# Optimization experiments

Hardware: AMD Instinct MI355X
Metric: run time of the kernel (lower is better)

## Reference

```python
import jax, jax.numpy as jnp
import numpy as np

B, S = 64, 256           # batch, seq_len
V, E = 50000, 256        # vocab, embedding dim
H, L = 256, 9            # lstm hidden, num labels


def setup_inputs() -> dict:
    key = jax.random.key(0)
    ks = jax.random.split(key, 12)
    inputs = jax.random.randint(ks[0], (B, S), 0, V, dtype=jnp.int32)
    attention_mask = jnp.ones((B, S), dtype=jnp.int32)
    label = jax.random.randint(ks[1], (B, S), 0, L, dtype=jnp.int32)
    emb = jax.random.normal(ks[2], (V, E), jnp.float32) * 0.02
    # LSTM weights, keras gate order: i, f, g(cell), o stacked along last axis
    W_fwd = jax.random.normal(ks[3], (E, 4 * H), jnp.float32) * 0.05
    U_fwd = jax.random.normal(ks[4], (H, 4 * H), jnp.float32) * 0.05
    b_fwd = jnp.zeros((4 * H,), jnp.float32)
    W_bwd = jax.random.normal(ks[5], (E, 4 * H), jnp.float32) * 0.05
    U_bwd = jax.random.normal(ks[6], (H, 4 * H), jnp.float32) * 0.05
    b_bwd = jnp.zeros((4 * H,), jnp.float32)
    W_dense = jax.random.normal(ks[7], (2 * H, L), jnp.float32) * 0.05
    b_dense = jnp.zeros((L,), jnp.float32)
    trans = jax.random.uniform(ks[8], (L, L), jnp.float32)  # tf.random.uniform init
    return dict(inputs=inputs, attention_mask=attention_mask, label=label,
                emb=emb, W_fwd=W_fwd, U_fwd=U_fwd, b_fwd=b_fwd,
                W_bwd=W_bwd, U_bwd=U_bwd, b_bwd=b_bwd,
                W_dense=W_dense, b_dense=b_dense, trans=trans)


def _lstm(x, W, U, b):
    # x: [B,S,E] -> h sequence [B,S,H]; keras default activations (sigmoid/tanh)
    Bx = x.shape[0]
    Hd = U.shape[0]
    xz = jnp.einsum('bse,ef->bsf', x, W) + b  # precompute input projection

    def step(carry, zt):
        h, c = carry
        z = zt + h @ U
        i, f, g, o = jnp.split(z, 4, axis=-1)
        c = jax.nn.sigmoid(f) * c + jax.nn.sigmoid(i) * jnp.tanh(g)
        h = jax.nn.sigmoid(o) * jnp.tanh(c)
        return (h, c), h

    init = (jnp.zeros((Bx, Hd), x.dtype), jnp.zeros((Bx, Hd), x.dtype))
    _, hs = jax.lax.scan(step, init, jnp.swapaxes(xz, 0, 1))
    return jnp.swapaxes(hs, 0, 1)


def _crf_log_likelihood(logits, tags, lengths, trans):
    # logits [B,S,L], tags [B,S] int, lengths [B] int, trans [L,L]
    Bx, Sx, Lx = logits.shape
    t_idx = jnp.arange(Sx)
    valid = (t_idx[None, :] < lengths[:, None]).astype(logits.dtype)  # [B,S]
    unary = jnp.take_along_axis(logits, tags[..., None], axis=-1)[..., 0]
    unary_score = jnp.sum(unary * valid, axis=1)
    pair_valid = (t_idx[None, :Sx - 1] < (lengths[:, None] - 1)).astype(logits.dtype)
    binary = trans[tags[:, :-1], tags[:, 1:]]
    binary_score = jnp.sum(binary * pair_valid, axis=1)

    # forward algorithm (log-space), masked so alpha is carried through padding
    alpha0 = logits[:, 0]  # [B,L]

    def step(alpha, inp):
        emit, m = inp  # emit [B,L], m [B] bool
        new = jax.nn.logsumexp(alpha[:, :, None] + trans[None], axis=1) + emit
        alpha = jnp.where(m[:, None], new, alpha)
        return alpha, None

    emits = jnp.swapaxes(logits[:, 1:], 0, 1)               # [S-1,B,L]
    masks = jnp.swapaxes(t_idx[None, 1:] < lengths[:, None], 0, 1)
    alpha, _ = jax.lax.scan(step, alpha0, (emits, masks))
    log_norm = jax.nn.logsumexp(alpha, axis=-1)
    return unary_score + binary_score - log_norm


def reference(inputs, attention_mask, label, emb, W_fwd, U_fwd, b_fwd,
              W_bwd, U_bwd, b_bwd, W_dense, b_dense, trans):
    x = emb[inputs]  # [B,S,E]; dropout is identity at inference (training=None)
    h_f = _lstm(x, W_fwd, U_fwd, b_fwd)
    h_b = _lstm(x[:, ::-1], W_bwd, U_bwd, b_bwd)[:, ::-1]
    h = jnp.concatenate([h_f, h_b], axis=-1)  # [B,S,2H]
    logits = h @ W_dense + b_dense            # [B,S,L]
    lengths = jnp.sum((attention_mask != 0).astype(jnp.int32), axis=1)
    log_likelihood = _crf_log_likelihood(logits, label, lengths, trans)
    return logits, log_likelihood, trans
```

## Files before the change

kernel.cpp:

```cpp
#include <hip/hip_runtime.h>
#include <hip/hip_fp16.h>

typedef _Float16 half2_t __attribute__((ext_vector_type(2)));
typedef unsigned int u32;

constexpr int Bn = 64, Sn = 256, Ln = 9;
constexpr int G4H = 1024;

constexpr size_t XZ_OFF   = 0;
constexpr size_t XZ_BYTES = (size_t)2 * Bn * Sn * G4H * 4;
constexpr size_t H_OFF    = XZ_OFF + XZ_BYTES;
constexpr size_t H_BYTES  = (size_t)Bn * Sn * 512 * 4;
constexpr size_t UPK_OFF  = H_OFF + H_BYTES;
constexpr size_t UPK_BYTES= (size_t)2 * 128 * G4H * 4;

__device__ __forceinline__ float sigf(float x) {
  return __fdividef(1.0f, 1.0f + __expf(-x));
}
__device__ __forceinline__ float tanhf_fast(float x) {
  x = fminf(fmaxf(x, -15.0f), 15.0f);
  float e = __expf(-2.0f * x);
  return __fdividef(1.0f - e, 1.0f + e);
}

#if __has_builtin(__builtin_amdgcn_fdot2)
__device__ __forceinline__ float FDOT2(half2_t a, half2_t b, float c) {
  return __builtin_amdgcn_fdot2(a, b, c, false);
}
#else
__device__ __forceinline__ float FDOT2(half2_t a, half2_t b, float c) {
  return c + (float)a.x * (float)b.x + (float)a.y * (float)b.y;
}
#endif

__device__ __forceinline__ half2_t H2(u32 w) { return __builtin_bit_cast(half2_t, w); }
__device__ __forceinline__ half2_t H2F(float f) { return __builtin_bit_cast(half2_t, f); }

__global__ void pack_u(const float* __restrict__ Uf, const float* __restrict__ Ub,
                       u32* __restrict__ upk) {
  int idx = blockIdx.x * 256 + threadIdx.x;
  if (idx >= 2 * 128 * 1024) return;
  int d  = idx >> 17;
  int kp = (idx >> 10) & 127;
  int j  = idx & 1023;
  const float* U = d ? Ub : Uf;
  _Float16 a = (_Float16)U[(size_t)(2 * kp) * 1024 + j];
  _Float16 b = (_Float16)U[(size_t)(2 * kp + 1) * 1024 + j];
  u32 pa = (u32)__builtin_bit_cast(unsigned short, a);
  u32 pb = (u32)__builtin_bit_cast(unsigned short, b);
  upk[idx] = pa | (pb << 16);
}

__global__ __launch_bounds__(256, 4)
void xz_gemm(const int* __restrict__ tok, const float* __restrict__ emb,
             const float* __restrict__ Wf, const float* __restrict__ biasf,
             const float* __restrict__ Wb, const float* __restrict__ biasb,
             float* __restrict__ xz) {
  __shared__ float As[32][64];
  __shared__ float Bs[32][128];
  __shared__ int toks[64];
  const int tid = threadIdx.x;
  const int mt = blockIdx.x, nt = blockIdx.y;
  const int d = nt >> 3;
  const float* W    = d ? Wb : Wf;
  const float* bias = d ? biasb : biasf;
  const int n0 = (nt & 7) * 128;
  const int r0 = mt * 64;
  if (tid < 64) toks[tid] = tok[r0 + tid];
  __syncthreads();
  const int tr = tid >> 4, tc = tid & 15;
  float acc[4][8];
#pragma unroll
  for (int j = 0; j < 8; ++j) {
    float bv = bias[n0 + tc * 8 + j];
#pragma unroll
    for (int i = 0; i < 4; ++i) acc[i][j] = bv;
  }
  const int ai = tid >> 2, kq = tid & 3;
  const int kb = tid >> 3, fb = tid & 7;
  for (int k0 = 0; k0 < 256; k0 += 32) {
    const float* ar = emb + (size_t)toks[ai] * 256 + k0 + kq * 8;
    float4 a0 = *(const float4*)ar;
    float4 a1 = *(const float4*)(ar + 4);
    As[kq * 8 + 0][ai] = a0.x; As[kq * 8 + 1][ai] = a0.y;
    As[kq * 8 + 2][ai] = a0.z; As[kq * 8 + 3][ai] = a0.w;
    As[kq * 8 + 4][ai] = a1.x; As[kq * 8 + 5][ai] = a1.y;
    As[kq * 8 + 6][ai] = a1.z; As[kq * 8 + 7][ai] = a1.w;
    const float* wr = W + (size_t)(k0 + kb) * 1024 + n0;
#pragma unroll
    for (int q = 0; q < 4; ++q)
      *(float4*)&Bs[kb][(fb + 8 * q) * 4] = *(const float4*)(wr + (fb + 8 * q) * 4);
    __syncthreads();
#pragma unroll
    for (int kk = 0; kk < 32; ++kk) {
      float4 a4 = *(const float4*)&As[kk][tr * 4];
      float4 b0 = *(const float4*)&Bs[kk][tc * 8];
      float4 b1 = *(const float4*)&Bs[kk][tc * 8 + 4];
      float av[4] = {a4.x, a4.y, a4.z, a4.w};
      float bv[8] = {b0.x, b0.y, b0.z, b0.w, b1.x, b1.y, b1.z, b1.w};
#pragma unroll
      for (int i = 0; i < 4; ++i)
#pragma unroll
        for (int j = 0; j < 8; ++j) acc[i][j] += av[i] * bv[j];
    }
    __syncthreads();
  }
#pragma unroll
  for (int i = 0; i < 4; ++i) {
    int r = r0 + tr * 4 + i;
    int bb_ = r >> 8, s = r & 255;
    float* dst = xz + ((size_t)(d * 64 + bb_) * 256 + s) * 1024 + n0 + tc * 8;
    float4 o0 = {acc[i][0], acc[i][1], acc[i][2], acc[i][3]};
    float4 o1 = {acc[i][4], acc[i][5], acc[i][6], acc[i][7]};
    *(float4*)dst = o0;
    *(float4*)(dst + 4) = o1;
  }
}

__global__ __launch_bounds__(1024)
void lstm_seq(const float* __restrict__ xz, const u32* __restrict__ upk,
              float* __restrict__ h_out) {
  const int seq = blockIdx.x;
  const int dir = seq >> 6;
  const int tid = threadIdx.x;

  __shared__ uint4 ul[8][1024];
  __shared__ float zbuf[1024];
  __shared__ __align__(16) u32 h2[128];

  const u32* ub = upk + (size_t)dir * 131072 + tid;

  float uu[96];
#pragma unroll
  for (int q = 0; q < 96; ++q)
    uu[q] = __builtin_bit_cast(float, ub[(size_t)q * 1024]);
#pragma unroll
  for (int q = 0; q < 96; ++q)
    asm volatile("" : "+v"(uu[q]));

#pragma unroll
  for (int s = 0; s < 8; ++s) {
    uint4 v;
    v.x = ub[(size_t)(96 + 4 * s + 0) * 1024];
    v.y = ub[(size_t)(96 + 4 * s + 1) * 1024];
    v.z = ub[(size_t)(96 + 4 * s + 2) * 1024];
    v.w = ub[(size_t)(96 + 4 * s + 3) * 1024];
    ul[s][tid] = v;
  }
  if (tid < 128) h2[tid] = 0u;

  float c = 0.0f;
  const int s0 = dir ? 255 : 0;
  const float* xzp = xz + (size_t)seq * 256 * 1024 + (size_t)s0 * 1024 + tid;
  const ptrdiff_t xstp = dir ? -1024 : 1024;
  float* hop = h_out + (size_t)(seq & 63) * 256 * 512 + (size_t)s0 * 512 + dir * 256 + (tid & 255);
  const ptrdiff_t hstp = dir ? -512 : 512;
  __syncthreads();

  float xc = *xzp;
  const float* xnp = xzp + xstp;

  for (int t = 0; t < 256; ++t) {
    float nx = *xnp;

    float acc = 0.0f;
#pragma unroll
    for (int s = 0; s < 24; ++s) {
      uint4 hh = *(const uint4*)&h2[4 * s];
      acc = FDOT2(H2(hh.x), H2F(uu[4 * s + 0]), acc);
      acc = FDOT2(H2(hh.y), H2F(uu[4 * s + 1]), acc);
      acc = FDOT2(H2(hh.z), H2F(uu[4 * s + 2]), acc);
      acc = FDOT2(H2(hh.w), H2F(uu[4 * s + 3]), acc);
    }
#pragma unroll
    for (int s = 0; s < 8; ++s) {
      uint4 hh = *(const uint4*)&h2[96 + 4 * s];
      uint4 va = ul[s][tid];
      acc = FDOT2(H2(hh.x), H2(va.x), acc);
      acc = FDOT2(H2(hh.y), H2(va.y), acc);
      acc = FDOT2(H2(hh.z), H2(va.z), acc);
      acc = FDOT2(H2(hh.w), H2(va.w), acc);
    }
    zbuf[tid] = acc + xc;
    __syncthreads();

    if (tid < 256) {
      float zi = zbuf[tid], zf = zbuf[tid + 256], zg = zbuf[tid + 512], zo = zbuf[tid + 768];
      c = sigf(zf) * c + sigf(zi) * tanhf_fast(zg);
      float h = sigf(zo) * tanhf_fast(c);
      *hop = h;
      ((_Float16*)h2)[tid] = (_Float16)h;
    }
    __syncthreads();

    xc = nx;
    xnp += xstp;
    hop += hstp;
  }
}

__global__ __launch_bounds__(256, 4)
void logits_k(const float* __restrict__ h_out, const float* __restrict__ Wd,
              const float* __restrict__ bd, float* __restrict__ out) {
  __shared__ float Ws[512 * 9];
  __shared__ float bs[16];
  const int tid = threadIdx.x;
  for (int i = tid; i < 4608; i += 256) Ws[i] = Wd[i];
  if (tid < 9) bs[tid] = bd[tid];
  __syncthreads();
  const int w = tid >> 6, lane = tid & 63;
  const int r0 = blockIdx.x * 16 + w * 4;
  for (int rr = 0; rr < 4; ++rr) {
    const int r = r0 + rr;
    const float* hp = h_out + (size_t)r * 512 + lane * 8;
    float4 h0 = *(const float4*)hp;
    float4 h1 = *(const float4*)(hp + 4);
    float hv[8] = {h0.x, h0.y, h0.z, h0.w, h1.x, h1.y, h1.z, h1.w};
    float outv = 0.0f;
#pragma unroll
    for (int l = 0; l < 9; ++l) {
      float p = 0.0f;
#pragma unroll
      for (int uu = 0; uu < 8; ++uu) p += hv[uu] * Ws[(lane * 8 + uu) * 9 + l];
      for (int off = 32; off; off >>= 1) p += __shfl_xor(p, off, 64);
      if (lane == l) outv = p;
    }
    if (lane < 9) out[(size_t)r * 9 + lane] = outv + bs[lane];
  }
}

__global__ void crf_k(const float* __restrict__ logits, const int* __restrict__ label,
                      const int* __restrict__ mask, const float* __restrict__ trans,
                      float* __restrict__ out_ll, float* __restrict__ out_trans) {
  const int b = blockIdx.x;
  const int lane = threadIdx.x;
  int cnt = 0;
#pragma unroll
  for (int q = 0; q < 4; ++q) cnt += (mask[b * 256 + lane + q * 64] != 0) ? 1 : 0;
  for (int off = 32; off; off >>= 1) cnt += __shfl_xor(cnt, off, 64);
  const int len = cnt;
  float un = 0.0f;
#pragma unroll
  for (int q = 0; q < 4; ++q) {
    int s = lane + q * 64;
    if (s < len) un += logits[((size_t)b * 256 + s) * 9 + label[b * 256 + s]];
  }
  for (int off = 32; off; off >>= 1) un += __shfl_xor(un, off, 64);
  float bin = 0.0f;
#pragma unroll
  for (int q = 0; q < 4; ++q) {
    int s = lane + q * 64;
    if (s < 255 && s < len - 1)
      bin += trans[label[b * 256 + s] * 9 + label[b * 256 + s + 1]];
  }
  for (int off = 32; off; off >>= 1) bin += __shfl_xor(bin, off, 64);
  float alpha = (lane < 9) ? logits[((size_t)b * 256) * 9 + lane] : -INFINITY;
  float tcol[9];
  if (lane < 9) {
#pragma unroll
    for (int i = 0; i < 9; ++i) tcol[i] = trans[i * 9 + lane];
  }
  for (int t = 1; t < 256; ++t) {
    float a[9];
#pragma unroll
    for (int i = 0; i < 9; ++i) a[i] = __shfl(alpha, i, 64);
    if (lane < 9) {
      float mx = a[0] + tcol[0];
#pragma unroll
      for (int i = 1; i < 9; ++i) mx = fmaxf(mx, a[i] + tcol[i]);
      float ssum = 0.0f;
#pragma unroll
      for (int i = 0; i < 9; ++i) ssum += __expf(a[i] + tcol[i] - mx);
      float nw = mx + __logf(ssum) + logits[((size_t)b * 256 + t) * 9 + lane];
      if (t < len) alpha = nw;
    }
  }
  float mx = alpha;
  for (int off = 32; off; off >>= 1) mx = fmaxf(mx, __shfl_xor(mx, off, 64));
  float e = __expf(alpha - mx);
  for (int off = 32; off; off >>= 1) e += __shfl_xor(e, off, 64);
  if (lane == 0) out_ll[b] = un + bin - (mx + __logf(e));
  if (b == 0) {
    for (int i = lane; i < 81; i += 64) out_trans[i] = trans[i];
  }
}

extern "C" void kernel_launch(void* const* d_in, const int* in_sizes, int n_in,
                              void* d_out, int out_size, void* d_ws, size_t ws_size,
                              hipStream_t stream) {
  (void)in_sizes; (void)n_in; (void)out_size; (void)ws_size;
  const int*   inputs = (const int*)d_in[0];
  const int*   amask  = (const int*)d_in[1];
  const int*   label  = (const int*)d_in[2];
  const float* emb    = (const float*)d_in[3];
  const float* Wf     = (const float*)d_in[4];
  const float* Uf     = (const float*)d_in[5];
  const float* bf     = (const float*)d_in[6];
  const float* Wb     = (const float*)d_in[7];
  const float* Ub     = (const float*)d_in[8];
  const float* bb     = (const float*)d_in[9];
  const float* Wd     = (const float*)d_in[10];
  const float* bd     = (const float*)d_in[11];
  const float* trans  = (const float*)d_in[12];

  char* ws = (char*)d_ws;
  float* xz    = (float*)(ws + XZ_OFF);
  float* h_out = (float*)(ws + H_OFF);
  u32*   upk   = (u32*)(ws + UPK_OFF);

  float* out      = (float*)d_out;
  float* out_ll   = out + (size_t)Bn * Sn * Ln;
  float* out_tr   = out_ll + Bn;

  pack_u<<<1024, 256, 0, stream>>>(Uf, Ub, upk);
  xz_gemm<<<dim3(256, 16), 256, 0, stream>>>(inputs, emb, Wf, bf, Wb, bb, xz);
  lstm_seq<<<128, 1024, 0, stream>>>(xz, upk, h_out);
  logits_k<<<1024, 256, 0, stream>>>(h_out, Wd, bd, out);
  crf_k<<<64, 64, 0, stream>>>(out, label, amask, trans, out_ll, out_tr);
}
```

Before: 780.8 us.

## Process two sequences per LSTM block and stream most of U from global/L2

The LSTM recurrence kernel now runs 64 blocks of 512 threads, each handling two batch sequences and two gate columns per thread. The recurrent weights are reused across both sequences. Only a quarter of U stays in LDS; the other three quarters are streamed from a repacked global buffer (likely L2-resident) every step, with double-buffered uint4 loads. This replaces the large register-resident weight array, cutting register pressure and halving the number of blocks. The cost is per-step global/L2 weight traffic on the serial critical path and less parallelism.

```diff
diff --git a/kernel.cpp b/kernel.cpp
--- a/kernel.cpp
+++ b/kernel.cpp
@@ -12,7 +12,9 @@
 constexpr size_t H_OFF    = XZ_OFF + XZ_BYTES;
 constexpr size_t H_BYTES  = (size_t)Bn * Sn * 512 * 4;
 constexpr size_t UPK_OFF  = H_OFF + H_BYTES;
-constexpr size_t UPK_BYTES= (size_t)2 * 128 * G4H * 4;
+constexpr size_t UPK_BYTES= (size_t)2 * 32 * G4H * 4;
+constexpr size_t USTR_OFF = UPK_OFF + UPK_BYTES;
+constexpr size_t USTR_BYTES = (size_t)2 * 6 * 4 * 1024 * 16;
 
 __device__ __forceinline__ float sigf(float x) {
   return __fdividef(1.0f, 1.0f + __expf(-x));
@@ -34,10 +36,9 @@
 #endif
 
 __device__ __forceinline__ half2_t H2(u32 w) { return __builtin_bit_cast(half2_t, w); }
-__device__ __forceinline__ half2_t H2F(float f) { return __builtin_bit_cast(half2_t, f); }
 
 __global__ void pack_u(const float* __restrict__ Uf, const float* __restrict__ Ub,
-                       u32* __restrict__ upk) {
+                       u32* __restrict__ upk, u32* __restrict__ ustr) {
   int idx = blockIdx.x * 256 + threadIdx.x;
   if (idx >= 2 * 128 * 1024) return;
   int d  = idx >> 17;
@@ -48,7 +49,14 @@
   _Float16 b = (_Float16)U[(size_t)(2 * kp + 1) * 1024 + j];
   u32 pa = (u32)__builtin_bit_cast(unsigned short, a);
   u32 pb = (u32)__builtin_bit_cast(unsigned short, b);
-  upk[idx] = pa | (pb << 16);
+  u32 v = pa | (pb << 16);
+  if (kp < 32) {
+    upk[((size_t)d * 32 + kp) * 1024 + j] = v;
+  } else {
+    int r = kp - 32;
+    int c = r >> 4, q = (r >> 2) & 3, e = r & 3;
+    ustr[((((size_t)d * 6 + c) * 4 + q) * 1024 + j) * 4 + e] = v;
+  }
 }
 
 __global__ __launch_bounds__(256, 4)
@@ -117,85 +125,130 @@
   }
 }
 
-__global__ __launch_bounds__(1024)
+__global__ __launch_bounds__(512)
 void lstm_seq(const float* __restrict__ xz, const u32* __restrict__ upk,
-              float* __restrict__ h_out) {
-  const int seq = blockIdx.x;
-  const int dir = seq >> 6;
+              const uint4* __restrict__ ustr, float* __restrict__ h_out) {
+  const int bid = blockIdx.x;
+  const int dir = bid >> 5;
+  const int g   = bid & 31;
+  const int b0  = 2 * g;
+  const int seq0 = dir * 64 + b0;
   const int tid = threadIdx.x;
-
-  __shared__ uint4 ul[8][1024];
-  __shared__ float zbuf[1024];
-  __shared__ __align__(16) u32 h2[128];
-
-  const u32* ub = upk + (size_t)dir * 131072 + tid;
-
-  float uu[96];
-#pragma unroll
-  for (int q = 0; q < 96; ++q)
-    uu[q] = __builtin_bit_cast(float, ub[(size_t)q * 1024]);
-#pragma unroll
-  for (int q = 0; q < 96; ++q)
-    asm volatile("" : "+v"(uu[q]));
-
-#pragma unroll
-  for (int s = 0; s < 8; ++s) {
-    uint4 v;
-    v.x = ub[(size_t)(96 + 4 * s + 0) * 1024];
-    v.y = ub[(size_t)(96 + 4 * s + 1) * 1024];
-    v.z = ub[(size_t)(96 + 4 * s + 2) * 1024];
-    v.w = ub[(size_t)(96 + 4 * s + 3) * 1024];
-    ul[s][tid] = v;
-  }
-  if (tid < 128) h2[tid] = 0u;
-
-  float c = 0.0f;
-  const int s0 = dir ? 255 : 0;
-  const float* xzp = xz + (size_t)seq * 256 * 1024 + (size_t)s0 * 1024 + tid;
-  const ptrdiff_t xstp = dir ? -1024 : 1024;
-  float* hop = h_out + (size_t)(seq & 63) * 256 * 512 + (size_t)s0 * 512 + dir * 256 + (tid & 255);
-  const ptrdiff_t hstp = dir ? -512 : 512;
+  const int colA = tid, colB = tid + 512;
+
+  __shared__ uint4 ul[16][512];
+  __shared__ float zbuf[2][1024];
+  __shared__ __align__(16) u32 h2[2][128];
+
+  const u32* ub = upk + (size_t)dir * 32768;
+#pragma unroll
+  for (int q = 0; q < 8; ++q) {
+    uint4 va, vb;
+    va.x = ub[(size_t)(4 * q + 0) * 1024 + colA];
+    va.y = ub[(size_t)(4 * q + 1) * 1024 + colA];
+    va.z = ub[(size_t)(4 * q + 2) * 1024 + colA];
+    va.w = ub[(size_t)(4 * q + 3) * 1024 + colA];
+    vb.x = ub[(size_t)(4 * q + 0) * 1024 + colB];
+    vb.y = ub[(size_t)(4 * q + 1) * 1024 + colB];
+    vb.z = ub[(size_t)(4 * q + 2) * 1024 + colB];
+    vb.w = ub[(size_t)(4 * q + 3) * 1024 + colB];
+    ul[q][tid] = va;
+    ul[8 + q][tid] = vb;
+  }
+  if (tid < 256) ((u32*)h2)[tid] = 0u;
+
+  const uint4* us = ustr + (size_t)dir * 6 * 4 * 1024;
+  const float* xzp0 = xz + (size_t)seq0 * 262144;
+  const float* xzp1 = xzp0 + 262144;
+  float* hop0 = h_out + (size_t)b0 * 131072 + dir * 256 + tid;
+  float* hop1 = hop0 + 131072;
+  float c0 = 0.0f, c1 = 0.0f;
   __syncthreads();
 
-  float xc = *xzp;
-  const float* xnp = xzp + xstp;
+  const int sfirst = dir ? 255 : 0;
+  float xA0 = xzp0[(size_t)sfirst * 1024 + colA];
+  float xB0 = xzp0[(size_t)sfirst * 1024 + colB];
+  float xA1 = xzp1[(size_t)sfirst * 1024 + colA];
+  float xB1 = xzp1[(size_t)sfirst * 1024 + colB];
 
   for (int t = 0; t < 256; ++t) {
-    float nx = *xnp;
-
-    float acc = 0.0f;
-#pragma unroll
-    for (int s = 0; s < 24; ++s) {
-      uint4 hh = *(const uint4*)&h2[4 * s];
-      acc = FDOT2(H2(hh.x), H2F(uu[4 * s + 0]), acc);
-      acc = FDOT2(H2(hh.y), H2F(uu[4 * s + 1]), acc);
-      acc = FDOT2(H2(hh.z), H2F(uu[4 * s + 2]), acc);
-      acc = FDOT2(H2(hh.w), H2F(uu[4 * s + 3]), acc);
-    }
-#pragma unroll
-    for (int s = 0; s < 8; ++s) {
-      uint4 hh = *(const uint4*)&h2[96 + 4 * s];
-      uint4 va = ul[s][tid];
-      acc = FDOT2(H2(hh.x), H2(va.x), acc);
-      acc = FDOT2(H2(hh.y), H2(va.y), acc);
-      acc = FDOT2(H2(hh.z), H2(va.z), acc);
-      acc = FDOT2(H2(hh.w), H2(va.w), acc);
-    }
-    zbuf[tid] = acc + xc;
+    const int scur  = dir ? (255 - t) : t;
+    const int snext = (t < 255) ? (dir ? (254 - t) : (t + 1)) : sfirst;
+
+    uint4 sA[2][4], sB[2][4];
+#pragma unroll
+    for (int q = 0; q < 4; ++q) {
+      sA[0][q] = us[(size_t)q * 1024 + colA];
+      sB[0][q] = us[(size_t)q * 1024 + colB];
+    }
+
+    float aA0 = xA0, aB0 = xB0, aA1 = xA1, aB1 = xB1;
+#pragma unroll
+    for (int q = 0; q < 8; ++q) {
+      uint4 h0 = *(const uint4*)&h2[0][4 * q];
+      uint4 h1 = *(const uint4*)&h2[1][4 * q];
+      uint4 va = ul[q][tid];
+      uint4 vb = ul[8 + q][tid];
+      aA0 = FDOT2(H2(h0.x), H2(va.x), aA0); aA0 = FDOT2(H2(h0.y), H2(va.y), aA0);
+      aA0 = FDOT2(H2(h0.z), H2(va.z), aA0); aA0 = FDOT2(H2(h0.w), H2(va.w), aA0);
+      aB0 = FDOT2(H2(h0.x), H2(vb.x), aB0); aB0 = FDOT2(H2(h0.y), H2(vb.y), aB0);
+      aB0 = FDOT2(H2(h0.z), H2(vb.z), aB0); aB0 = FDOT2(H2(h0.w), H2(vb.w), aB0);
+      aA1 = FDOT2(H2(h1.x), H2(va.x), aA1); aA1 = FDOT2(H2(h1.y), H2(va.y), aA1);
+      aA1 = FDOT2(H2(h1.z), H2(va.z), aA1); aA1 = FDOT2(H2(h1.w), H2(va.w), aA1);
+      aB1 = FDOT2(H2(h1.x), H2(vb.x), aB1); aB1 = FDOT2(H2(h1.y), H2(vb.y), aB1);
+      aB1 = FDOT2(H2(h1.z), H2(vb.z), aB1); aB1 = FDOT2(H2(h1.w), H2(vb.w), aB1);
+    }
+#pragma unroll
+    for (int cc = 0; cc < 6; ++cc) {
+      const int cur = cc & 1, nxt = cur ^ 1;
+      if (cc < 5) {
+#pragma unroll
+        for (int q = 0; q < 4; ++q) {
+          sA[nxt][q] = us[(size_t)((cc + 1) * 4 + q) * 1024 + colA];
+          sB[nxt][q] = us[(size_t)((cc + 1) * 4 + q) * 1024 + colB];
+        }
+      }
+#pragma unroll
+      for (int q = 0; q < 4; ++q) {
+        const int pb = 32 + 16 * cc + 4 * q;
+        uint4 h0 = *(const uint4*)&h2[0][pb];
+        uint4 h1 = *(const uint4*)&h2[1][pb];
+        uint4 va = sA[cur][q];
+        uint4 vb = sB[cur][q];
+        aA0 = FDOT2(H2(h0.x), H2(va.x), aA0); aA0 = FDOT2(H2(h0.y), H2(va.y), aA0);
+        aA0 = FDOT2(H2(h0.z), H2(va.z), aA0); aA0 = FDOT2(H2(h0.w), H2(va.w), aA0);
+        aB0 = FDOT2(H2(h0.x), H2(vb.x), aB0); aB0 = FDOT2(H2(h0.y), H2(vb.y), aB0);
+        aB0 = FDOT2(H2(h0.z), H2(vb.z), aB0); aB0 = FDOT2(H2(h0.w), H2(vb.w), aB0);
+        aA1 = FDOT2(H2(h1.x), H2(va.x), aA1); aA1 = FDOT2(H2(h1.y), H2(va.y), aA1);
+        aA1 = FDOT2(H2(h1.z), H2(va.z), aA1); aA1 = FDOT2(H2(h1.w), H2(va.w), aA1);
+        aB1 = FDOT2(H2(h1.x), H2(vb.x), aB1); aB1 = FDOT2(H2(h1.y), H2(vb.y), aB1);
+        aB1 = FDOT2(H2(h1.z), H2(vb.z), aB1); aB1 = FDOT2(H2(h1.w), H2(vb.w), aB1);
+      }
+    }
+    zbuf[0][colA] = aA0; zbuf[0][colB] = aB0;
+    zbuf[1][colA] = aA1; zbuf[1][colB] = aB1;
+    float nA0 = xzp0[(size_t)snext * 1024 + colA];
+    float nB0 = xzp0[(size_t)snext * 1024 + colB];
+    float nA1 = xzp1[(size_t)snext * 1024 + colA];
+    float nB1 = xzp1[(size_t)snext * 1024 + colB];
     __syncthreads();
 
     if (tid < 256) {
-      float zi = zbuf[tid], zf = zbuf[tid + 256], zg = zbuf[tid + 512], zo = zbuf[tid + 768];
-      c = sigf(zf) * c + sigf(zi) * tanhf_fast(zg);
-      float h = sigf(zo) * tanhf_fast(c);
-      *hop = h;
-      ((_Float16*)h2)[tid] = (_Float16)h;
+      float zi = zbuf[0][tid], zf = zbuf[0][tid + 256];
+      float zg = zbuf[0][tid + 512], zo = zbuf[0][tid + 768];
+      c0 = sigf(zf) * c0 + sigf(zi) * tanhf_fast(zg);
+      float h0v = sigf(zo) * tanhf_fast(c0);
+      hop0[(size_t)scur * 512] = h0v;
+      ((_Float16*)&h2[0][0])[tid] = (_Float16)h0v;
+      zi = zbuf[1][tid]; zf = zbuf[1][tid + 256];
+      zg = zbuf[1][tid + 512]; zo = zbuf[1][tid + 768];
+      c1 = sigf(zf) * c1 + sigf(zi) * tanhf_fast(zg);
+      float h1v = sigf(zo) * tanhf_fast(c1);
+      hop1[(size_t)scur * 512] = h1v;
+      ((_Float16*)&h2[1][0])[tid] = (_Float16)h1v;
     }
     __syncthreads();
-
-    xc = nx;
-    xnp += xstp;
-    hop += hstp;
+    xA0 = nA0; xB0 = nB0; xA1 = nA1; xB1 = nB1;
   }
 }
 
@@ -307,14 +360,15 @@
   float* xz    = (float*)(ws + XZ_OFF);
   float* h_out = (float*)(ws + H_OFF);
   u32*   upk   = (u32*)(ws + UPK_OFF);
+  u32*   ustr  = (u32*)(ws + USTR_OFF);
 
   float* out      = (float*)d_out;
   float* out_ll   = out + (size_t)Bn * Sn * Ln;
   float* out_tr   = out_ll + Bn;
 
-  pack_u<<<1024, 256, 0, stream>>>(Uf, Ub, upk);
+  pack_u<<<1024, 256, 0, stream>>>(Uf, Ub, upk, ustr);
   xz_gemm<<<dim3(256, 16), 256, 0, stream>>>(inputs, emb, Wf, bf, Wb, bb, xz);
-  lstm_seq<<<128, 1024, 0, stream>>>(xz, upk, h_out);
+  lstm_seq<<<64, 512, 0, stream>>>(xz, upk, (const uint4*)ustr, h_out);
   logits_k<<<1024, 256, 0, stream>>>(h_out, Wd, bd, out);
   crf_k<<<64, 64, 0, stream>>>(out, label, amask, trans, out_ll, out_tr);
 }
```

After: 1.131 ms. +44.8%, slower.
